# Kernel optimization log

Measured on AMD Instinct MI355X. Metric: run time of the kernel, lower is better.

The kernel has to match this reference:

```python
import jax, jax.numpy as jnp
import numpy as np

BATCH, IN_WIDTH, OUT_FEATURES, FAN_IN = 512, 4096, 4096, 128

def setup_inputs() -> dict:
    key = jax.random.key(0)
    k1, k2, k3, k4 = jax.random.split(key, 4)
    input = jax.random.normal(k1, (BATCH, IN_WIDTH), dtype=jnp.float32)
    weight = jax.random.normal(k2, (OUT_FEATURES, FAN_IN), dtype=jnp.float32)
    bias = jax.random.normal(k3, (OUT_FEATURES,), dtype=jnp.float32)
    indx_seqs = jax.random.randint(k4, (OUT_FEATURES, FAN_IN), 0, IN_WIDTH, dtype=jnp.int64)
    return {"input": input, "weight": weight, "bias": bias, "indx_seqs": indx_seqs}

def reference(input, weight, bias, indx_seqs):
    # gather: (B, out_features, fan_in)
    gathered = input[:, indx_seqs]
    # elementwise mul with weight (out_features, fan_in), reduce over fan_in
    return jnp.einsum('bof,of->bo', gathered, weight) + bias
```

## Files before the change

### kernel.cpp

```cpp
#include <hip/hip_runtime.h>
#include <hip/hip_bf16.h>

#define BATCH    512
#define IN_WIDTH 4096
#define OUT_F    4096
#define FAN_IN   128
#define BCHUNK   16
#define NBG      (BATCH / BCHUNK)
#define OBLK     512
#define NOG      (OUT_F / OBLK)

typedef float    v2f __attribute__((ext_vector_type(2)));
typedef uint32_t v4u __attribute__((ext_vector_type(4)));

__global__ __launch_bounds__(256) void k_transpose_in(const float* __restrict__ in,
                                                      uint16_t* __restrict__ inTg) {
  __shared__ float tile[32][33];
  const int jt = blockIdx.x * 32;
  const int bt = blockIdx.y * 32;
  const int tx = threadIdx.x;
  const int ty = threadIdx.y;
#pragma unroll
  for (int r = 0; r < 32; r += 8) {
    tile[ty + r][tx] = in[(size_t)(bt + ty + r) * IN_WIDTH + (jt + tx)];
  }
  __syncthreads();
#pragma unroll
  for (int r = 0; r < 32; r += 8) {
    const int b = bt + tx;
    const int j = jt + ty + r;
    __hip_bfloat16 hv = __float2bfloat16(tile[tx][ty + r]);
    inTg[((size_t)(b >> 4) * IN_WIDTH + j) * BCHUNK + (b & 15)] =
        *reinterpret_cast<const uint16_t*>(&hv);
  }
}

__global__ __launch_bounds__(256) void k_pack(const int* __restrict__ idx,
                                              const float* __restrict__ weight,
                                              uint2* __restrict__ pk) {
  const int i = blockIdx.x * 256 + threadIdx.x;
  uint2 e;
  e.x = (uint32_t)idx[i];
  e.y = __float_as_uint(weight[i]);
  pk[i] = e;
}

__global__ __launch_bounds__(1024, 4) void k_gather_lds(const uint16_t* __restrict__ inTg,
                                                        const uint2* __restrict__ pk,
                                                        const float* __restrict__ bias,
                                                        float* __restrict__ out) {
  extern __shared__ char lds[];
  const int og = blockIdx.x;
  const int bg = blockIdx.y;
  const int t  = threadIdx.x;

  {
    const v4u* __restrict__ src =
        reinterpret_cast<const v4u*>(inTg + (size_t)bg * IN_WIDTH * BCHUNK);
    v4u* dst = reinterpret_cast<v4u*>(lds);
#pragma unroll
    for (int i = 0; i < 8; ++i) dst[i * 1024 + t] = src[i * 1024 + t];
  }
  __syncthreads();

  const int wv = t >> 6;
  const int l  = t & 63;
  const int o  = og * OBLK + wv * 32 + (l >> 1);
  const int p  = l & 1;

  const uint32_t sb = (uint32_t)(size_t)lds + (uint32_t)(p * 16);

  const uint4* __restrict__ pko =
      reinterpret_cast<const uint4*>(pk + (size_t)o * FAN_IN);

  v2f a0 = {0.f, 0.f}, a1 = {0.f, 0.f}, a2 = {0.f, 0.f}, a3 = {0.f, 0.f};

#define DSREAD(d, jj) \
  asm volatile("ds_read_b128 %0, %1" : "=v"(d) : "v"(sb + ((jj) << 5)))

#define WAIT4() do { asm volatile("s_waitcnt lgkmcnt(4)" ::: "memory"); \
                     __builtin_amdgcn_sched_barrier(0); } while (0)
#define WAIT0() do { asm volatile("s_waitcnt lgkmcnt(0)" ::: "memory"); \
                     __builtin_amdgcn_sched_barrier(0); } while (0)

#define CONSUME(v, wbits)                                              \
  do {                                                                 \
    const float wf_ = __uint_as_float(wbits);                          \
    v2f w2_; w2_[0] = wf_; w2_[1] = wf_;                               \
    v2f x0_, x1_, x2_, x3_;                                            \
    x0_[0] = __uint_as_float((v).x << 16);                             \
    x0_[1] = __uint_as_float((v).x & 0xffff0000u);                     \
    x1_[0] = __uint_as_float((v).y << 16);                             \
    x1_[1] = __uint_as_float((v).y & 0xffff0000u);                     \
    x2_[0] = __uint_as_float((v).z << 16);                             \
    x2_[1] = __uint_as_float((v).z & 0xffff0000u);                     \
    x3_[0] = __uint_as_float((v).w << 16);                             \
    x3_[1] = __uint_as_float((v).w & 0xffff0000u);                     \
    a0 += x0_ * w2_; a1 += x1_ * w2_; a2 += x2_ * w2_; a3 += x3_ * w2_;\
  } while (0)

  uint4 q0a = pko[0], q0b = pko[1];
  uint4 q1a = pko[2], q1b = pko[3];
  uint4 q2a = pko[4], q2b = pko[5];
  uint4 q3a = pko[6], q3b = pko[7];

  v4u vA0, vA1, vA2, vA3, vB0, vB1, vB2, vB3;
  uint32_t wA0, wA1, wA2, wA3, wB0, wB1, wB2, wB3;

  DSREAD(vA0, q0a.x); DSREAD(vA1, q0a.z); DSREAD(vA2, q0b.x); DSREAD(vA3, q0b.z);
  wA0 = q0a.y; wA1 = q0a.w; wA2 = q0b.y; wA3 = q0b.w;

#define STEP(Cc, QI0, QI1, QR0, QR1,                                   \
             VC0, VC1, VC2, VC3, WC0, WC1, WC2, WC3,                   \
             VI0, VI1, VI2, VI3, WI0, WI1, WI2, WI3)                   \
  do {                                                                 \
    DSREAD(VI0, QI0.x); DSREAD(VI1, QI0.z);                            \
    DSREAD(VI2, QI1.x); DSREAD(VI3, QI1.z);                            \
    WI0 = QI0.y; WI1 = QI0.w; WI2 = QI1.y; WI3 = QI1.w;                \
    {                                                                  \
      const int gn_ = ((Cc) + 4 > 31) ? 31 : ((Cc) + 4);               \
      QR0 = pko[2 * gn_];                                              \
      QR1 = pko[2 * gn_ + 1];                                          \
    }                                                                  \
    WAIT4();                                                           \
    CONSUME(VC0, WC0); CONSUME(VC1, WC1);                              \
    CONSUME(VC2, WC2); CONSUME(VC3, WC3);                              \
  } while (0)

#define STEP_A(Cc, QI0, QI1, QR0, QR1)  \
  STEP(Cc, QI0, QI1, QR0, QR1,                                           \
       vA0, vA1, vA2, vA3, wA0, wA1, wA2, wA3,                           \
       vB0, vB1, vB2, vB3, wB0, wB1, wB2, wB3)
#define STEP_B(Cc, QI0, QI1, QR0, QR1)   \
  STEP(Cc, QI0, QI1, QR0, QR1,                                           \
       vB0, vB1, vB2, vB3, wB0, wB1, wB2, wB3,                           \
       vA0, vA1, vA2, vA3, wA0, wA1, wA2, wA3)

#pragma unroll 1
  for (int cb = 0; cb < 28; cb += 4) {
    STEP_A(cb + 0, q1a, q1b, q0a, q0b);
    STEP_B(cb + 1, q2a, q2b, q1a, q1b);
    STEP_A(cb + 2, q3a, q3b, q2a, q2b);
    STEP_B(cb + 3, q0a, q0b, q3a, q3b);
  }
  STEP_A(28, q1a, q1b, q0a, q0b);
  STEP_B(29, q2a, q2b, q1a, q1b);
  STEP_A(30, q3a, q3b, q2a, q2b);
  WAIT0();
  CONSUME(vB0, wB0); CONSUME(vB1, wB1); CONSUME(vB2, wB2); CONSUME(vB3, wB3);

  const float bz = bias[o];
  const float r[8] = {a0[0], a0[1], a1[0], a1[1], a2[0], a2[1], a3[0], a3[1]};
  const size_t obase = (size_t)(bg * BCHUNK + p * 8) * OUT_F + o;
#pragma unroll
  for (int i = 0; i < 8; ++i) out[obase + (size_t)i * OUT_F] = r[i] + bz;

#undef STEP_B
#undef STEP_A
#undef STEP
#undef CONSUME
#undef WAIT4
#undef WAIT0
#undef DSREAD
}

extern "C" void kernel_launch(void* const* d_in, const int* in_sizes, int n_in,
                              void* d_out, int out_size, void* d_ws, size_t ws_size,
                              hipStream_t stream) {
  const float* input  = (const float*)d_in[0];
  const float* weight = (const float*)d_in[1];
  const float* bias   = (const float*)d_in[2];
  const int*   idx    = (const int*)d_in[3];
  float* out = (float*)d_out;

  uint16_t* inTg = (uint16_t*)d_ws;
  uint2*    pk   = (uint2*)((char*)d_ws + 4u * 1024 * 1024);

  dim3 tblk(32, 8);
  k_transpose_in<<<dim3(IN_WIDTH / 32, BATCH / 32), tblk, 0, stream>>>(input, inTg);
  k_pack<<<dim3(OUT_F * FAN_IN / 256), dim3(256), 0, stream>>>(idx, weight, pk);
  k_gather_lds<<<dim3(NOG, NBG), dim3(1024), IN_WIDTH * BCHUNK * 2, stream>>>(
      inTg, pk, bias, out);
}
```

Baseline: 37.79 us.

## Shrink batch chunk to 4 with one output per thread and 64-bit LDS reads

Cuts the batch chunk held in LDS from 16 to 4 rows, so each block stages 32 KB instead of 128 KB and more blocks can be resident per CU. Each thread now computes one output feature over 4 batch rows with ds_read_b64 gathers, instead of two lanes splitting 16 rows with 128-bit reads. The transpose kernel writes packed 4-element bf16 groups as uint2 stores. The tradeoff is that each packed index/weight stream is reread by four times as many blocks (128 batch groups instead of 32), which raises global/L2 traffic for the pk array.

Measured after the change: 94.77 us. 151% more time.

```diff
diff --git a/kernel.cpp b/kernel.cpp
--- a/kernel.cpp
+++ b/kernel.cpp
@@ -5,12 +5,13 @@
 #define IN_WIDTH 4096
 #define OUT_F    4096
 #define FAN_IN   128
-#define BCHUNK   16
+#define BCHUNK   4
 #define NBG      (BATCH / BCHUNK)
 #define OBLK     512
 #define NOG      (OUT_F / OBLK)
 
 typedef float    v2f __attribute__((ext_vector_type(2)));
+typedef uint32_t v2u __attribute__((ext_vector_type(2)));
 typedef uint32_t v4u __attribute__((ext_vector_type(4)));
 
 __global__ __launch_bounds__(256) void k_transpose_in(const float* __restrict__ in,
@@ -18,21 +19,26 @@
   __shared__ float tile[32][33];
   const int jt = blockIdx.x * 32;
   const int bt = blockIdx.y * 32;
-  const int tx = threadIdx.x;
-  const int ty = threadIdx.y;
+  const int t  = threadIdx.x;
+  const int tx = t & 31;
+  const int ty = t >> 5;
 #pragma unroll
   for (int r = 0; r < 32; r += 8) {
     tile[ty + r][tx] = in[(size_t)(bt + ty + r) * IN_WIDTH + (jt + tx)];
   }
   __syncthreads();
+  const int jl   = t & 31;
+  const int bgrp = t >> 5;
+  uint32_t d[2];
 #pragma unroll
-  for (int r = 0; r < 32; r += 8) {
-    const int b = bt + tx;
-    const int j = jt + ty + r;
-    __hip_bfloat16 hv = __float2bfloat16(tile[tx][ty + r]);
-    inTg[((size_t)(b >> 4) * IN_WIDTH + j) * BCHUNK + (b & 15)] =
-        *reinterpret_cast<const uint16_t*>(&hv);
+  for (int h = 0; h < 2; ++h) {
+    __hip_bfloat16 h0 = __float2bfloat16(tile[bgrp * 4 + 2 * h][jl]);
+    __hip_bfloat16 h1 = __float2bfloat16(tile[bgrp * 4 + 2 * h + 1][jl]);
+    d[h] = (uint32_t)(*reinterpret_cast<uint16_t*>(&h0)) |
+           ((uint32_t)(*reinterpret_cast<uint16_t*>(&h1)) << 16);
   }
+  uint2* dst = reinterpret_cast<uint2*>(inTg);
+  dst[((size_t)((bt >> 2) + bgrp)) * IN_WIDTH + (jt + jl)] = make_uint2(d[0], d[1]);
 }
 
 __global__ __launch_bounds__(256) void k_pack(const int* __restrict__ idx,
@@ -45,10 +51,10 @@
   pk[i] = e;
 }
 
-__global__ __launch_bounds__(1024, 4) void k_gather_lds(const uint16_t* __restrict__ inTg,
-                                                        const uint2* __restrict__ pk,
-                                                        const float* __restrict__ bias,
-                                                        float* __restrict__ out) {
+__global__ __launch_bounds__(512, 8) void k_gather_lds(const uint16_t* __restrict__ inTg,
+                                                       const uint2* __restrict__ pk,
+                                                       const float* __restrict__ bias,
+                                                       float* __restrict__ out) {
   extern __shared__ char lds[];
   const int og = blockIdx.x;
   const int bg = blockIdx.y;
@@ -59,24 +65,20 @@
         reinterpret_cast<const v4u*>(inTg + (size_t)bg * IN_WIDTH * BCHUNK);
     v4u* dst = reinterpret_cast<v4u*>(lds);
 #pragma unroll
-    for (int i = 0; i < 8; ++i) dst[i * 1024 + t] = src[i * 1024 + t];
+    for (int i = 0; i < 4; ++i) dst[i * 512 + t] = src[i * 512 + t];
   }
   __syncthreads();
 
-  const int wv = t >> 6;
-  const int l  = t & 63;
-  const int o  = og * OBLK + wv * 32 + (l >> 1);
-  const int p  = l & 1;
-
-  const uint32_t sb = (uint32_t)(size_t)lds + (uint32_t)(p * 16);
+  const int o = og * OBLK + t;
+  const uint32_t sb = (uint32_t)(size_t)lds;
 
   const uint4* __restrict__ pko =
       reinterpret_cast<const uint4*>(pk + (size_t)o * FAN_IN);
 
-  v2f a0 = {0.f, 0.f}, a1 = {0.f, 0.f}, a2 = {0.f, 0.f}, a3 = {0.f, 0.f};
+  v2f a0 = {0.f, 0.f}, a1 = {0.f, 0.f};
 
 #define DSREAD(d, jj) \
-  asm volatile("ds_read_b128 %0, %1" : "=v"(d) : "v"(sb + ((jj) << 5)))
+  asm volatile("ds_read_b64 %0, %1" : "=v"(d) : "v"(sb + ((jj) << 3)))
 
 #define WAIT4() do { asm volatile("s_waitcnt lgkmcnt(4)" ::: "memory"); \
                      __builtin_amdgcn_sched_barrier(0); } while (0)
@@ -87,76 +89,55 @@
   do {                                                                 \
     const float wf_ = __uint_as_float(wbits);                          \
     v2f w2_; w2_[0] = wf_; w2_[1] = wf_;                               \
-    v2f x0_, x1_, x2_, x3_;                                            \
-    x0_[0] = __uint_as_float((v).x << 16);                             \
-    x0_[1] = __uint_as_float((v).x & 0xffff0000u);                     \
-    x1_[0] = __uint_as_float((v).y << 16);                             \
-    x1_[1] = __uint_as_float((v).y & 0xffff0000u);                     \
-    x2_[0] = __uint_as_float((v).z << 16);                             \
-    x2_[1] = __uint_as_float((v).z & 0xffff0000u);                     \
-    x3_[0] = __uint_as_float((v).w << 16);                             \
-    x3_[1] = __uint_as_float((v).w & 0xffff0000u);                     \
-    a0 += x0_ * w2_; a1 += x1_ * w2_; a2 += x2_ * w2_; a3 += x3_ * w2_;\
+    v2f x0_, x1_;                                                      \
+    x0_[0] = __uint_as_float((v)[0] << 16);                            \
+    x0_[1] = __uint_as_float((v)[0] & 0xffff0000u);                    \
+    x1_[0] = __uint_as_float((v)[1] << 16);                            \
+    x1_[1] = __uint_as_float((v)[1] & 0xffff0000u);                    \
+    a0 += x0_ * w2_; a1 += x1_ * w2_;                                  \
   } while (0)
 
   uint4 q0a = pko[0], q0b = pko[1];
   uint4 q1a = pko[2], q1b = pko[3];
   uint4 q2a = pko[4], q2b = pko[5];
-  uint4 q3a = pko[6], q3b = pko[7];
 
-  v4u vA0, vA1, vA2, vA3, vB0, vB1, vB2, vB3;
-  uint32_t wA0, wA1, wA2, wA3, wB0, wB1, wB2, wB3;
+  v2u A0, A1, A2, A3, B0, B1, B2, B3;
 
-  DSREAD(vA0, q0a.x); DSREAD(vA1, q0a.z); DSREAD(vA2, q0b.x); DSREAD(vA3, q0b.z);
-  wA0 = q0a.y; wA1 = q0a.w; wA2 = q0b.y; wA3 = q0b.w;
+  DSREAD(A0, q0a.x); DSREAD(A1, q0a.z); DSREAD(A2, q0b.x); DSREAD(A3, q0b.z);
 
-#define STEP(Cc, QI0, QI1, QR0, QR1,                                   \
-             VC0, VC1, VC2, VC3, WC0, WC1, WC2, WC3,                   \
-             VI0, VI1, VI2, VI3, WI0, WI1, WI2, WI3)                   \
+#define STEP(Cc, QIa, QIb, QCa, QCb, VC0, VC1, VC2, VC3, VI0, VI1, VI2, VI3) \
   do {                                                                 \
-    DSREAD(VI0, QI0.x); DSREAD(VI1, QI0.z);                            \
-    DSREAD(VI2, QI1.x); DSREAD(VI3, QI1.z);                            \
-    WI0 = QI0.y; WI1 = QI0.w; WI2 = QI1.y; WI3 = QI1.w;                \
+    DSREAD(VI0, QIa.x); DSREAD(VI1, QIa.z);                            \
+    DSREAD(VI2, QIb.x); DSREAD(VI3, QIb.z);                            \
+    WAIT4();                                                           \
+    CONSUME(VC0, QCa.y); CONSUME(VC1, QCa.w);                          \
+    CONSUME(VC2, QCb.y); CONSUME(VC3, QCb.w);                          \
     {                                                                  \
-      const int gn_ = ((Cc) + 4 > 31) ? 31 : ((Cc) + 4);               \
-      QR0 = pko[2 * gn_];                                              \
-      QR1 = pko[2 * gn_ + 1];                                          \
+      const int gn_ = ((Cc) + 3 > 31) ? 31 : ((Cc) + 3);               \
+      QCa = pko[2 * gn_];                                              \
+      QCb = pko[2 * gn_ + 1];                                          \
     }                                                                  \
-    WAIT4();                                                           \
-    CONSUME(VC0, WC0); CONSUME(VC1, WC1);                              \
-    CONSUME(VC2, WC2); CONSUME(VC3, WC3);                              \
   } while (0)
 
-#define STEP_A(Cc, QI0, QI1, QR0, QR1)  \
-  STEP(Cc, QI0, QI1, QR0, QR1,                                           \
-       vA0, vA1, vA2, vA3, wA0, wA1, wA2, wA3,                           \
-       vB0, vB1, vB2, vB3, wB0, wB1, wB2, wB3)
-#define STEP_B(Cc, QI0, QI1, QR0, QR1)   \
-  STEP(Cc, QI0, QI1, QR0, QR1,                                           \
-       vB0, vB1, vB2, vB3, wB0, wB1, wB2, wB3,                           \
-       vA0, vA1, vA2, vA3, wA0, wA1, wA2, wA3)
-
 #pragma unroll 1
-  for (int cb = 0; cb < 28; cb += 4) {
-    STEP_A(cb + 0, q1a, q1b, q0a, q0b);
-    STEP_B(cb + 1, q2a, q2b, q1a, q1b);
-    STEP_A(cb + 2, q3a, q3b, q2a, q2b);
-    STEP_B(cb + 3, q0a, q0b, q3a, q3b);
+  for (int cb = 0; cb < 30; cb += 6) {
+    STEP(cb + 0, q1a, q1b, q0a, q0b, A0, A1, A2, A3, B0, B1, B2, B3);
+    STEP(cb + 1, q2a, q2b, q1a, q1b, B0, B1, B2, B3, A0, A1, A2, A3);
+    STEP(cb + 2, q0a, q0b, q2a, q2b, A0, A1, A2, A3, B0, B1, B2, B3);
+    STEP(cb + 3, q1a, q1b, q0a, q0b, B0, B1, B2, B3, A0, A1, A2, A3);
+    STEP(cb + 4, q2a, q2b, q1a, q1b, A0, A1, A2, A3, B0, B1, B2, B3);
+    STEP(cb + 5, q0a, q0b, q2a, q2b, B0, B1, B2, B3, A0, A1, A2, A3);
   }
-  STEP_A(28, q1a, q1b, q0a, q0b);
-  STEP_B(29, q2a, q2b, q1a, q1b);
-  STEP_A(30, q3a, q3b, q2a, q2b);
+  STEP(30, q1a, q1b, q0a, q0b, A0, A1, A2, A3, B0, B1, B2, B3);
   WAIT0();
-  CONSUME(vB0, wB0); CONSUME(vB1, wB1); CONSUME(vB2, wB2); CONSUME(vB3, wB3);
+  CONSUME(B0, q1a.y); CONSUME(B1, q1a.w); CONSUME(B2, q1b.y); CONSUME(B3, q1b.w);
 
   const float bz = bias[o];
-  const float r[8] = {a0[0], a0[1], a1[0], a1[1], a2[0], a2[1], a3[0], a3[1]};
-  const size_t obase = (size_t)(bg * BCHUNK + p * 8) * OUT_F + o;
+  const float r[4] = {a0[0], a0[1], a1[0], a1[1]};
+  const size_t obase = (size_t)bg * BCHUNK * OUT_F + o;
 #pragma unroll
-  for (int i = 0; i < 8; ++i) out[obase + (size_t)i * OUT_F] = r[i] + bz;
+  for (int i = 0; i < 4; ++i) out[obase + (size_t)i * OUT_F] = r[i] + bz;
 
-#undef STEP_B
-#undef STEP_A
 #undef STEP
 #undef CONSUME
 #undef WAIT4
@@ -176,9 +157,8 @@
   uint16_t* inTg = (uint16_t*)d_ws;
   uint2*    pk   = (uint2*)((char*)d_ws + 4u * 1024 * 1024);
 
-  dim3 tblk(32, 8);
-  k_transpose_in<<<dim3(IN_WIDTH / 32, BATCH / 32), tblk, 0, stream>>>(input, inTg);
+  k_transpose_in<<<dim3(IN_WIDTH / 32, BATCH / 32), dim3(256), 0, stream>>>(input, inTg);
   k_pack<<<dim3(OUT_F * FAN_IN / 256), dim3(256), 0, stream>>>(idx, weight, pk);
-  k_gather_lds<<<dim3(NOG, NBG), dim3(1024), IN_WIDTH * BCHUNK * 2, stream>>>(
+  k_gather_lds<<<dim3(NOG, NBG), dim3(512), IN_WIDTH * BCHUNK * 2, stream>>>(
       inTg, pk, bias, out);
 }
```

## Split gather waves between LDS reads and direct global loads

Applied to the files above, without the earlier changes.

Waves 0-6 of each block keep gathering input rows from LDS as before. Waves 7-15 instead gather them directly from global memory, which goes through the L1/L2 caches, using a simple one-step prefetch loop. The goal is to ease LDS bandwidth and bank-conflict pressure by sending part of the random-gather traffic through the vector memory path. The risk is that the global-load waves see higher latency and become stragglers, and the whole block is still staged into LDS.

Result: slower. 72.79 us (+92.6%).

```diff
diff --git a/kernel.cpp b/kernel.cpp
--- a/kernel.cpp
+++ b/kernel.cpp
@@ -9,6 +9,7 @@
 #define NBG      (BATCH / BCHUNK)
 #define OBLK     512
 #define NOG      (OUT_F / OBLK)
+#define WL       7
 
 typedef float    v2f __attribute__((ext_vector_type(2)));
 typedef uint32_t v4u __attribute__((ext_vector_type(4)));
@@ -44,44 +45,6 @@
   e.y = __float_as_uint(weight[i]);
   pk[i] = e;
 }
-
-__global__ __launch_bounds__(1024, 4) void k_gather_lds(const uint16_t* __restrict__ inTg,
-                                                        const uint2* __restrict__ pk,
-                                                        const float* __restrict__ bias,
-                                                        float* __restrict__ out) {
-  extern __shared__ char lds[];
-  const int og = blockIdx.x;
-  const int bg = blockIdx.y;
-  const int t  = threadIdx.x;
-
-  {
-    const v4u* __restrict__ src =
-        reinterpret_cast<const v4u*>(inTg + (size_t)bg * IN_WIDTH * BCHUNK);
-    v4u* dst = reinterpret_cast<v4u*>(lds);
-#pragma unroll
-    for (int i = 0; i < 8; ++i) dst[i * 1024 + t] = src[i * 1024 + t];
-  }
-  __syncthreads();
-
-  const int wv = t >> 6;
-  const int l  = t & 63;
-  const int o  = og * OBLK + wv * 32 + (l >> 1);
-  const int p  = l & 1;
-
-  const uint32_t sb = (uint32_t)(size_t)lds + (uint32_t)(p * 16);
-
-  const uint4* __restrict__ pko =
-      reinterpret_cast<const uint4*>(pk + (size_t)o * FAN_IN);
-
-  v2f a0 = {0.f, 0.f}, a1 = {0.f, 0.f}, a2 = {0.f, 0.f}, a3 = {0.f, 0.f};
-
-#define DSREAD(d, jj) \
-  asm volatile("ds_read_b128 %0, %1" : "=v"(d) : "v"(sb + ((jj) << 5)))
-
-#define WAIT4() do { asm volatile("s_waitcnt lgkmcnt(4)" ::: "memory"); \
-                     __builtin_amdgcn_sched_barrier(0); } while (0)
-#define WAIT0() do { asm volatile("s_waitcnt lgkmcnt(0)" ::: "memory"); \
-                     __builtin_amdgcn_sched_barrier(0); } while (0)
 
 #define CONSUME(v, wbits)                                              \
   do {                                                                 \
@@ -99,16 +62,54 @@
     a0 += x0_ * w2_; a1 += x1_ * w2_; a2 += x2_ * w2_; a3 += x3_ * w2_;\
   } while (0)
 
-  uint4 q0a = pko[0], q0b = pko[1];
-  uint4 q1a = pko[2], q1b = pko[3];
-  uint4 q2a = pko[4], q2b = pko[5];
-  uint4 q3a = pko[6], q3b = pko[7];
-
-  v4u vA0, vA1, vA2, vA3, vB0, vB1, vB2, vB3;
-  uint32_t wA0, wA1, wA2, wA3, wB0, wB1, wB2, wB3;
-
-  DSREAD(vA0, q0a.x); DSREAD(vA1, q0a.z); DSREAD(vA2, q0b.x); DSREAD(vA3, q0b.z);
-  wA0 = q0a.y; wA1 = q0a.w; wA2 = q0b.y; wA3 = q0b.w;
+__global__ __launch_bounds__(1024, 4) void k_gather_hyb(const uint16_t* __restrict__ inTg,
+                                                        const uint2* __restrict__ pk,
+                                                        const float* __restrict__ bias,
+                                                        float* __restrict__ out) {
+  extern __shared__ char lds[];
+  const int og = blockIdx.x;
+  const int bg = blockIdx.y;
+  const int t  = threadIdx.x;
+
+  {
+    const v4u* __restrict__ src =
+        reinterpret_cast<const v4u*>(inTg + (size_t)bg * IN_WIDTH * BCHUNK);
+    v4u* dst = reinterpret_cast<v4u*>(lds);
+#pragma unroll
+    for (int i = 0; i < 8; ++i) dst[i * 1024 + t] = src[i * 1024 + t];
+  }
+  __syncthreads();
+
+  const int wv = t >> 6;
+  const int l  = t & 63;
+  const int p  = l & 1;
+
+  v2f a0 = {0.f, 0.f}, a1 = {0.f, 0.f}, a2 = {0.f, 0.f}, a3 = {0.f, 0.f};
+  int o;
+
+  if (wv < WL) {
+    o = og * OBLK + wv * 32 + (l >> 1);
+    const uint32_t sb = (uint32_t)(size_t)lds + (uint32_t)(p * 16);
+    const uint4* __restrict__ pko =
+        reinterpret_cast<const uint4*>(pk + (size_t)o * FAN_IN);
+
+#define DSREAD(d, jj) \
+  asm volatile("ds_read_b128 %0, %1" : "=v"(d) : "v"(sb + ((jj) << 5)))
+#define WAIT4() do { asm volatile("s_waitcnt lgkmcnt(4)" ::: "memory"); \
+                     __builtin_amdgcn_sched_barrier(0); } while (0)
+#define WAIT0() do { asm volatile("s_waitcnt lgkmcnt(0)" ::: "memory"); \
+                     __builtin_amdgcn_sched_barrier(0); } while (0)
+
+    uint4 q0a = pko[0], q0b = pko[1];
+    uint4 q1a = pko[2], q1b = pko[3];
+    uint4 q2a = pko[4], q2b = pko[5];
+    uint4 q3a = pko[6], q3b = pko[7];
+
+    v4u vA0, vA1, vA2, vA3, vB0, vB1, vB2, vB3;
+    uint32_t wA0, wA1, wA2, wA3, wB0, wB1, wB2, wB3;
+
+    DSREAD(vA0, q0a.x); DSREAD(vA1, q0a.z); DSREAD(vA2, q0b.x); DSREAD(vA3, q0b.z);
+    wA0 = q0a.y; wA1 = q0a.w; wA2 = q0b.y; wA3 = q0b.w;
 
 #define STEP(Cc, QI0, QI1, QR0, QR1,                                   \
              VC0, VC1, VC2, VC3, WC0, WC1, WC2, WC3,                   \
@@ -126,42 +127,65 @@
     CONSUME(VC0, WC0); CONSUME(VC1, WC1);                              \
     CONSUME(VC2, WC2); CONSUME(VC3, WC3);                              \
   } while (0)
-
-#define STEP_A(Cc, QI0, QI1, QR0, QR1)  \
+#define STEP_A(Cc, QI0, QI1, QR0, QR1)                                   \
   STEP(Cc, QI0, QI1, QR0, QR1,                                           \
        vA0, vA1, vA2, vA3, wA0, wA1, wA2, wA3,                           \
        vB0, vB1, vB2, vB3, wB0, wB1, wB2, wB3)
-#define STEP_B(Cc, QI0, QI1, QR0, QR1)   \
+#define STEP_B(Cc, QI0, QI1, QR0, QR1)                                   \
   STEP(Cc, QI0, QI1, QR0, QR1,                                           \
        vB0, vB1, vB2, vB3, wB0, wB1, wB2, wB3,                           \
        vA0, vA1, vA2, vA3, wA0, wA1, wA2, wA3)
 
 #pragma unroll 1
-  for (int cb = 0; cb < 28; cb += 4) {
-    STEP_A(cb + 0, q1a, q1b, q0a, q0b);
-    STEP_B(cb + 1, q2a, q2b, q1a, q1b);
-    STEP_A(cb + 2, q3a, q3b, q2a, q2b);
-    STEP_B(cb + 3, q0a, q0b, q3a, q3b);
-  }
-  STEP_A(28, q1a, q1b, q0a, q0b);
-  STEP_B(29, q2a, q2b, q1a, q1b);
-  STEP_A(30, q3a, q3b, q2a, q2b);
-  WAIT0();
-  CONSUME(vB0, wB0); CONSUME(vB1, wB1); CONSUME(vB2, wB2); CONSUME(vB3, wB3);
+    for (int cb = 0; cb < 28; cb += 4) {
+      STEP_A(cb + 0, q1a, q1b, q0a, q0b);
+      STEP_B(cb + 1, q2a, q2b, q1a, q1b);
+      STEP_A(cb + 2, q3a, q3b, q2a, q2b);
+      STEP_B(cb + 3, q0a, q0b, q3a, q3b);
+    }
+    STEP_A(28, q1a, q1b, q0a, q0b);
+    STEP_B(29, q2a, q2b, q1a, q1b);
+    STEP_A(30, q3a, q3b, q2a, q2b);
+    WAIT0();
+    CONSUME(vB0, wB0); CONSUME(vB1, wB1); CONSUME(vB2, wB2); CONSUME(vB3, wB3);
+#undef STEP_B
+#undef STEP_A
+#undef STEP
+#undef WAIT4
+#undef WAIT0
+#undef DSREAD
+  } else {
+    o = og * OBLK + WL * 32 + (wv - WL) * 32 + (l >> 1);
+    const uint16_t* __restrict__ gbase =
+        inTg + (size_t)bg * IN_WIDTH * BCHUNK + p * 8;
+    const uint4* __restrict__ pko =
+        reinterpret_cast<const uint4*>(pk + (size_t)o * FAN_IN);
+
+#define GLD(jj) (*reinterpret_cast<const uint4*>(gbase + (size_t)(jj) * BCHUNK))
+
+    uint4 qa = pko[0], qb = pko[1];
+    uint4 va0 = GLD(qa.x), va1 = GLD(qa.z), va2 = GLD(qb.x), va3 = GLD(qb.z);
+#pragma unroll 1
+    for (int g = 0; g < 31; ++g) {
+      const uint4 qn0 = pko[2 * g + 2];
+      const uint4 qn1 = pko[2 * g + 3];
+      const uint4 vb0 = GLD(qn0.x), vb1 = GLD(qn0.z);
+      const uint4 vb2 = GLD(qn1.x), vb3 = GLD(qn1.z);
+      CONSUME(va0, qa.y); CONSUME(va1, qa.w);
+      CONSUME(va2, qb.y); CONSUME(va3, qb.w);
+      qa = qn0; qb = qn1;
+      va0 = vb0; va1 = vb1; va2 = vb2; va3 = vb3;
+    }
+    CONSUME(va0, qa.y); CONSUME(va1, qa.w);
+    CONSUME(va2, qb.y); CONSUME(va3, qb.w);
+#undef GLD
+  }
 
   const float bz = bias[o];
   const float r[8] = {a0[0], a0[1], a1[0], a1[1], a2[0], a2[1], a3[0], a3[1]};
   const size_t obase = (size_t)(bg * BCHUNK + p * 8) * OUT_F + o;
 #pragma unroll
   for (int i = 0; i < 8; ++i) out[obase + (size_t)i * OUT_F] = r[i] + bz;
-
-#undef STEP_B
-#undef STEP_A
-#undef STEP
-#undef CONSUME
-#undef WAIT4
-#undef WAIT0
-#undef DSREAD
 }
 
 extern "C" void kernel_launch(void* const* d_in, const int* in_sizes, int n_in,
@@ -179,6 +203,6 @@
   dim3 tblk(32, 8);
   k_transpose_in<<<dim3(IN_WIDTH / 32, BATCH / 32), tblk, 0, stream>>>(input, inTg);
   k_pack<<<dim3(OUT_F * FAN_IN / 256), dim3(256), 0, stream>>>(idx, weight, pk);
-  k_gather_lds<<<dim3(NOG, NBG), dim3(1024), IN_WIDTH * BCHUNK * 2, stream>>>(
+  k_gather_hyb<<<dim3(NOG, NBG), dim3(1024), IN_WIDTH * BCHUNK * 2, stream>>>(
       inTg, pk, bias, out);
 }
```

## Split output features between LDS-gather and direct global-gather wave paths

Applied to the files above, without the earlier changes.

Each 1024-thread block now runs two kinds of waves. Half the waves handle the first 2048 outputs with the existing LDS-based bf16 gather. The other half handle the remaining outputs by gathering full batch rows straight from a new batch-contiguous bf16 copy of the input in global memory, writing transposed results that a new kernel transposes back. The intent is to balance LDS bandwidth against global/L2 bandwidth so both paths run at once. The cost is an extra input layout write, an extra output transpose kernel with its round trip, and a smaller k_pack.

New measurement: 43.58 us. 15.3% more time.

```diff
diff --git a/kernel.cpp b/kernel.cpp
--- a/kernel.cpp
+++ b/kernel.cpp
@@ -7,14 +7,14 @@
 #define FAN_IN   128
 #define BCHUNK   16
 #define NBG      (BATCH / BCHUNK)
-#define OBLK     512
-#define NOG      (OUT_F / OBLK)
+#define O_SPLIT  2048
 
 typedef float    v2f __attribute__((ext_vector_type(2)));
 typedef uint32_t v4u __attribute__((ext_vector_type(4)));
 
 __global__ __launch_bounds__(256) void k_transpose_in(const float* __restrict__ in,
-                                                      uint16_t* __restrict__ inTg) {
+                                                      uint16_t* __restrict__ inTg,
+                                                      uint16_t* __restrict__ inTf) {
   __shared__ float tile[32][33];
   const int jt = blockIdx.x * 32;
   const int bt = blockIdx.y * 32;
@@ -30,8 +30,9 @@
     const int b = bt + tx;
     const int j = jt + ty + r;
     __hip_bfloat16 hv = __float2bfloat16(tile[tx][ty + r]);
-    inTg[((size_t)(b >> 4) * IN_WIDTH + j) * BCHUNK + (b & 15)] =
-        *reinterpret_cast<const uint16_t*>(&hv);
+    const uint16_t u = *reinterpret_cast<const uint16_t*>(&hv);
+    inTg[((size_t)(b >> 4) * IN_WIDTH + j) * BCHUNK + (b & 15)] = u;
+    inTf[(size_t)j * BATCH + b] = u;
   }
 }
 
@@ -45,70 +46,71 @@
   pk[i] = e;
 }
 
-__global__ __launch_bounds__(1024, 4) void k_gather_lds(const uint16_t* __restrict__ inTg,
-                                                        const uint2* __restrict__ pk,
-                                                        const float* __restrict__ bias,
-                                                        float* __restrict__ out) {
-  extern __shared__ char lds[];
-  const int og = blockIdx.x;
-  const int bg = blockIdx.y;
-  const int t  = threadIdx.x;
-
-  {
-    const v4u* __restrict__ src =
-        reinterpret_cast<const v4u*>(inTg + (size_t)bg * IN_WIDTH * BCHUNK);
-    v4u* dst = reinterpret_cast<v4u*>(lds);
-#pragma unroll
-    for (int i = 0; i < 8; ++i) dst[i * 1024 + t] = src[i * 1024 + t];
-  }
-  __syncthreads();
-
-  const int wv = t >> 6;
-  const int l  = t & 63;
-  const int o  = og * OBLK + wv * 32 + (l >> 1);
-  const int p  = l & 1;
-
-  const uint32_t sb = (uint32_t)(size_t)lds + (uint32_t)(p * 16);
-
-  const uint4* __restrict__ pko =
-      reinterpret_cast<const uint4*>(pk + (size_t)o * FAN_IN);
-
-  v2f a0 = {0.f, 0.f}, a1 = {0.f, 0.f}, a2 = {0.f, 0.f}, a3 = {0.f, 0.f};
-
-#define DSREAD(d, jj) \
-  asm volatile("ds_read_b128 %0, %1" : "=v"(d) : "v"(sb + ((jj) << 5)))
-
-#define WAIT4() do { asm volatile("s_waitcnt lgkmcnt(4)" ::: "memory"); \
-                     __builtin_amdgcn_sched_barrier(0); } while (0)
-#define WAIT0() do { asm volatile("s_waitcnt lgkmcnt(0)" ::: "memory"); \
-                     __builtin_amdgcn_sched_barrier(0); } while (0)
-
 #define CONSUME(v, wbits)                                              \
   do {                                                                 \
     const float wf_ = __uint_as_float(wbits);                          \
     v2f w2_; w2_[0] = wf_; w2_[1] = wf_;                               \
     v2f x0_, x1_, x2_, x3_;                                            \
-    x0_[0] = __uint_as_float((v).x << 16);                             \
-    x0_[1] = __uint_as_float((v).x & 0xffff0000u);                     \
-    x1_[0] = __uint_as_float((v).y << 16);                             \
-    x1_[1] = __uint_as_float((v).y & 0xffff0000u);                     \
-    x2_[0] = __uint_as_float((v).z << 16);                             \
-    x2_[1] = __uint_as_float((v).z & 0xffff0000u);                     \
-    x3_[0] = __uint_as_float((v).w << 16);                             \
-    x3_[1] = __uint_as_float((v).w & 0xffff0000u);                     \
+    x0_[0] = __uint_as_float((v)[0] << 16);                            \
+    x0_[1] = __uint_as_float((v)[0] & 0xffff0000u);                    \
+    x1_[0] = __uint_as_float((v)[1] << 16);                            \
+    x1_[1] = __uint_as_float((v)[1] & 0xffff0000u);                    \
+    x2_[0] = __uint_as_float((v)[2] << 16);                            \
+    x2_[1] = __uint_as_float((v)[2] & 0xffff0000u);                    \
+    x3_[0] = __uint_as_float((v)[3] << 16);                            \
+    x3_[1] = __uint_as_float((v)[3] & 0xffff0000u);                    \
     a0 += x0_ * w2_; a1 += x1_ * w2_; a2 += x2_ * w2_; a3 += x3_ * w2_;\
   } while (0)
 
-  uint4 q0a = pko[0], q0b = pko[1];
-  uint4 q1a = pko[2], q1b = pko[3];
-  uint4 q2a = pko[4], q2b = pko[5];
-  uint4 q3a = pko[6], q3b = pko[7];
-
-  v4u vA0, vA1, vA2, vA3, vB0, vB1, vB2, vB3;
-  uint32_t wA0, wA1, wA2, wA3, wB0, wB1, wB2, wB3;
-
-  DSREAD(vA0, q0a.x); DSREAD(vA1, q0a.z); DSREAD(vA2, q0b.x); DSREAD(vA3, q0b.z);
-  wA0 = q0a.y; wA1 = q0a.w; wA2 = q0b.y; wA3 = q0b.w;
+__global__ __launch_bounds__(1024, 1) void k_gather_hyb2(
+    const uint16_t* __restrict__ inTg, const uint16_t* __restrict__ inTf,
+    const uint2* __restrict__ pk, const int* __restrict__ idx,
+    const float* __restrict__ weight, const float* __restrict__ bias,
+    float* __restrict__ out, float* __restrict__ outT) {
+  extern __shared__ char lds[];
+  const int blk = blockIdx.x;
+  const int og  = blk & 7;
+  const int bg  = blk >> 3;
+  const int t   = threadIdx.x;
+
+  {
+    const v4u* __restrict__ src =
+        reinterpret_cast<const v4u*>(inTg + (size_t)bg * IN_WIDTH * BCHUNK);
+    v4u* dst = reinterpret_cast<v4u*>(lds);
+#pragma unroll
+    for (int i = 0; i < 8; ++i) dst[i * 1024 + t] = src[i * 1024 + t];
+  }
+  __syncthreads();
+
+  const int wv = t >> 6;
+  const int l  = t & 63;
+
+  v2f a0 = {0.f, 0.f}, a1 = {0.f, 0.f}, a2 = {0.f, 0.f}, a3 = {0.f, 0.f};
+
+  if (wv < 8) {
+    const int p = l & 1;
+    const int o = og * 256 + wv * 32 + (l >> 1);
+    const uint32_t sb = (uint32_t)(size_t)lds + (uint32_t)(p * 16);
+    const uint4* __restrict__ pko =
+        reinterpret_cast<const uint4*>(pk + (size_t)o * FAN_IN);
+
+#define DSREAD(d, jj) \
+  asm volatile("ds_read_b128 %0, %1" : "=v"(d) : "v"(sb + ((jj) << 5)))
+#define WAIT4() do { asm volatile("s_waitcnt lgkmcnt(4)" ::: "memory"); \
+                     __builtin_amdgcn_sched_barrier(0); } while (0)
+#define WAIT0() do { asm volatile("s_waitcnt lgkmcnt(0)" ::: "memory"); \
+                     __builtin_amdgcn_sched_barrier(0); } while (0)
+
+    uint4 q0a = pko[0], q0b = pko[1];
+    uint4 q1a = pko[2], q1b = pko[3];
+    uint4 q2a = pko[4], q2b = pko[5];
+    uint4 q3a = pko[6], q3b = pko[7];
+
+    v4u vA0, vA1, vA2, vA3, vB0, vB1, vB2, vB3;
+    uint32_t wA0, wA1, wA2, wA3, wB0, wB1, wB2, wB3;
+
+    DSREAD(vA0, q0a.x); DSREAD(vA1, q0a.z); DSREAD(vA2, q0b.x); DSREAD(vA3, q0b.z);
+    wA0 = q0a.y; wA1 = q0a.w; wA2 = q0b.y; wA3 = q0b.w;
 
 #define STEP(Cc, QI0, QI1, QR0, QR1,                                   \
              VC0, VC1, VC2, VC3, WC0, WC1, WC2, WC3,                   \
@@ -126,42 +128,105 @@
     CONSUME(VC0, WC0); CONSUME(VC1, WC1);                              \
     CONSUME(VC2, WC2); CONSUME(VC3, WC3);                              \
   } while (0)
-
-#define STEP_A(Cc, QI0, QI1, QR0, QR1)  \
+#define STEP_A(Cc, QI0, QI1, QR0, QR1)                                   \
   STEP(Cc, QI0, QI1, QR0, QR1,                                           \
        vA0, vA1, vA2, vA3, wA0, wA1, wA2, wA3,                           \
        vB0, vB1, vB2, vB3, wB0, wB1, wB2, wB3)
-#define STEP_B(Cc, QI0, QI1, QR0, QR1)   \
+#define STEP_B(Cc, QI0, QI1, QR0, QR1)                                   \
   STEP(Cc, QI0, QI1, QR0, QR1,                                           \
        vB0, vB1, vB2, vB3, wB0, wB1, wB2, wB3,                           \
        vA0, vA1, vA2, vA3, wA0, wA1, wA2, wA3)
 
 #pragma unroll 1
-  for (int cb = 0; cb < 28; cb += 4) {
-    STEP_A(cb + 0, q1a, q1b, q0a, q0b);
-    STEP_B(cb + 1, q2a, q2b, q1a, q1b);
-    STEP_A(cb + 2, q3a, q3b, q2a, q2b);
-    STEP_B(cb + 3, q0a, q0b, q3a, q3b);
-  }
-  STEP_A(28, q1a, q1b, q0a, q0b);
-  STEP_B(29, q2a, q2b, q1a, q1b);
-  STEP_A(30, q3a, q3b, q2a, q2b);
-  WAIT0();
-  CONSUME(vB0, wB0); CONSUME(vB1, wB1); CONSUME(vB2, wB2); CONSUME(vB3, wB3);
-
-  const float bz = bias[o];
-  const float r[8] = {a0[0], a0[1], a1[0], a1[1], a2[0], a2[1], a3[0], a3[1]};
-  const size_t obase = (size_t)(bg * BCHUNK + p * 8) * OUT_F + o;
-#pragma unroll
-  for (int i = 0; i < 8; ++i) out[obase + (size_t)i * OUT_F] = r[i] + bz;
-
+    for (int cb = 0; cb < 28; cb += 4) {
+      STEP_A(cb + 0, q1a, q1b, q0a, q0b);
+      STEP_B(cb + 1, q2a, q2b, q1a, q1b);
+      STEP_A(cb + 2, q3a, q3b, q2a, q2b);
+      STEP_B(cb + 3, q0a, q0b, q3a, q3b);
+    }
+    STEP_A(28, q1a, q1b, q0a, q0b);
+    STEP_B(29, q2a, q2b, q1a, q1b);
+    STEP_A(30, q3a, q3b, q2a, q2b);
+    WAIT0();
+    CONSUME(vB0, wB0); CONSUME(vB1, wB1); CONSUME(vB2, wB2); CONSUME(vB3, wB3);
 #undef STEP_B
 #undef STEP_A
 #undef STEP
-#undef CONSUME
 #undef WAIT4
 #undef WAIT0
 #undef DSREAD
+
+    const float bz = bias[o];
+    const float r[8] = {a0[0], a0[1], a1[0], a1[1], a2[0], a2[1], a3[0], a3[1]};
+    const size_t obase = (size_t)(bg * BCHUNK + p * 8) * OUT_F + o;
+#pragma unroll
+    for (int i = 0; i < 8; ++i) out[obase + (size_t)i * OUT_F] = r[i] + bz;
+
+  } else {
+    const int o = __builtin_amdgcn_readfirstlane(O_SPLIT + blk * 8 + (wv - 8));
+    const int*   __restrict__ idxo = idx + (size_t)o * FAN_IN;
+    const float* __restrict__ wo   = weight + (size_t)o * FAN_IN;
+    const uint32_t voff = (uint32_t)l * 16u;
+
+#define GISSUE(S, jj)                                                        \
+  do {                                                                       \
+    const uint32_t va_ = ((uint32_t)(jj) << 10) + voff;                      \
+    asm volatile("global_load_dwordx4 %0, %1, %2"                            \
+                 : "=&v"(S) : "v"(va_), "s"(inTf));                          \
+  } while (0)
+#define WAITV(n) do { asm volatile("s_waitcnt vmcnt(" #n ")" ::: "memory");  \
+                      __builtin_amdgcn_sched_barrier(0); } while (0)
+
+    v4u S0, S1, S2, S3;
+    int   j0 = idxo[0], j1 = idxo[1], j2 = idxo[2], j3 = idxo[3];
+    float w0 = wo[0],   w1 = wo[1],   w2 = wo[2],   w3 = wo[3];
+
+    GISSUE(S0, j0); GISSUE(S1, j1); GISSUE(S2, j2); GISSUE(S3, j3);
+
+#pragma unroll 1
+    for (int c = 0; c < 124; c += 4) {
+      const int   jn0 = idxo[c + 4], jn1 = idxo[c + 5];
+      const int   jn2 = idxo[c + 6], jn3 = idxo[c + 7];
+      const float wn0 = wo[c + 4],   wn1 = wo[c + 5];
+      const float wn2 = wo[c + 6],   wn3 = wo[c + 7];
+      WAITV(3); CONSUME(S0, __float_as_uint(w0)); GISSUE(S0, jn0); w0 = wn0;
+      WAITV(3); CONSUME(S1, __float_as_uint(w1)); GISSUE(S1, jn1); w1 = wn1;
+      WAITV(3); CONSUME(S2, __float_as_uint(w2)); GISSUE(S2, jn2); w2 = wn2;
+      WAITV(3); CONSUME(S3, __float_as_uint(w3)); GISSUE(S3, jn3); w3 = wn3;
+    }
+    WAITV(3); CONSUME(S0, __float_as_uint(w0));
+    WAITV(2); CONSUME(S1, __float_as_uint(w1));
+    WAITV(1); CONSUME(S2, __float_as_uint(w2));
+    WAITV(0); CONSUME(S3, __float_as_uint(w3));
+#undef WAITV
+#undef GISSUE
+
+    const float bz = bias[o];
+    float4 r0 = make_float4(a0[0] + bz, a0[1] + bz, a1[0] + bz, a1[1] + bz);
+    float4 r1 = make_float4(a2[0] + bz, a2[1] + bz, a3[0] + bz, a3[1] + bz);
+    float4* dst =
+        reinterpret_cast<float4*>(outT + (size_t)(o - O_SPLIT) * BATCH + l * 8);
+    dst[0] = r0;
+    dst[1] = r1;
+  }
+}
+
+__global__ __launch_bounds__(256) void k_transpose_out(const float* __restrict__ outT,
+                                                       float* __restrict__ out) {
+  __shared__ float tile[32][33];
+  const int ot = blockIdx.x * 32;
+  const int bt = blockIdx.y * 32;
+  const int tx = threadIdx.x;
+  const int ty = threadIdx.y;
+#pragma unroll
+  for (int r = 0; r < 32; r += 8) {
+    tile[ty + r][tx] = outT[(size_t)(ot + ty + r) * BATCH + (bt + tx)];
+  }
+  __syncthreads();
+#pragma unroll
+  for (int r = 0; r < 32; r += 8) {
+    out[(size_t)(bt + ty + r) * OUT_F + (O_SPLIT + ot + tx)] = tile[tx][ty + r];
+  }
 }
 
 extern "C" void kernel_launch(void* const* d_in, const int* in_sizes, int n_in,
@@ -174,11 +239,14 @@
   float* out = (float*)d_out;
 
   uint16_t* inTg = (uint16_t*)d_ws;
-  uint2*    pk   = (uint2*)((char*)d_ws + 4u * 1024 * 1024);
+  uint16_t* inTf = (uint16_t*)((char*)d_ws + 4u * 1024 * 1024);
+  uint2*    pk   = (uint2*)((char*)d_ws + 8u * 1024 * 1024);
+  float*    outT = (float*)((char*)d_ws + 10u * 1024 * 1024);
 
   dim3 tblk(32, 8);
-  k_transpose_in<<<dim3(IN_WIDTH / 32, BATCH / 32), tblk, 0, stream>>>(input, inTg);
-  k_pack<<<dim3(OUT_F * FAN_IN / 256), dim3(256), 0, stream>>>(idx, weight, pk);
-  k_gather_lds<<<dim3(NOG, NBG), dim3(1024), IN_WIDTH * BCHUNK * 2, stream>>>(
-      inTg, pk, bias, out);
-}
+  k_transpose_in<<<dim3(IN_WIDTH / 32, BATCH / 32), tblk, 0, stream>>>(input, inTg, inTf);
+  k_pack<<<dim3(O_SPLIT * FAN_IN / 256), dim3(256), 0, stream>>>(idx, weight, pk);
+  k_gather_hyb2<<<dim3(8 * NBG), dim3(1024), IN_WIDTH * BCHUNK * 2, stream>>>(
+      inTg, inTf, pk, idx, weight, bias, out, outT);
+  k_transpose_out<<<dim3(O_SPLIT / 32, BATCH / 32), tblk, 0, stream>>>(outT, out);
+}
```
